# Kernel optimization log

Hardware: AMD Instinct MI355X
Metric: run time of the kernel (lower is better)

Reference implementation:

```python
import jax, jax.numpy as jnp
import numpy as np

UNITS = [100, 80, 50, 30]
D_IN = 64


def _lstm_layer(x, Wx, Wh, b):
    # x: [B, T, D]; Wx: [D, 4u]; Wh: [u, 4u]; b: [4u]
    B = x.shape[0]
    u = Wh.shape[0]
    # precompute input contribution for all timesteps: [B, T, 4u]
    xg = jnp.einsum('btd,dg->btg', x, Wx) + b

    def step(carry, xg_t):
        h, c = carry
        g = xg_t + h @ Wh                      # [B, 4u]
        i, f, cbar, o = jnp.split(g, 4, axis=-1)
        i = jax.nn.sigmoid(i)
        f = jax.nn.sigmoid(f)
        o = jax.nn.sigmoid(o)
        c = f * c + i * jnp.tanh(cbar)
        h = o * jnp.tanh(c)
        return (h, c), h

    init = (jnp.zeros((B, u), x.dtype), jnp.zeros((B, u), x.dtype))
    (h_final, _), hs = jax.lax.scan(step, init, jnp.swapaxes(xg, 0, 1))
    return jnp.swapaxes(hs, 0, 1), h_final  # [B, T, u], [B, u]


def setup_inputs() -> dict:
    key = jax.random.key(0)
    ks = jax.random.split(key, 16)
    B, T = 256, 1024
    inp = {"sequence": jax.random.normal(ks[0], (B, T, D_IN), dtype=jnp.float32)}
    d_in = D_IN
    for li, u in enumerate(UNITS):
        s_x = 1.0 / np.sqrt(d_in)
        s_h = 1.0 / np.sqrt(u)
        inp[f"Wx{li}"] = jax.random.normal(ks[1 + 3 * li], (d_in, 4 * u), dtype=jnp.float32) * s_x
        inp[f"Wh{li}"] = jax.random.normal(ks[2 + 3 * li], (u, 4 * u), dtype=jnp.float32) * s_h
        inp[f"b{li}"] = jnp.zeros((4 * u,), dtype=jnp.float32)
        d_in = u
    inp["W_out"] = jax.random.normal(ks[13], (UNITS[-1], 1), dtype=jnp.float32) / np.sqrt(UNITS[-1])
    inp["b_out"] = jnp.zeros((1,), dtype=jnp.float32)
    return inp


def reference(sequence, Wx0, Wh0, b0, Wx1, Wh1, b1, Wx2, Wh2, b2, Wx3, Wh3, b3, W_out, b_out):
    # 4 stacked LSTM layers; dropout is identity at inference.
    x, _ = _lstm_layer(sequence, Wx0, Wh0, b0)   # [B, T, 100]
    x, _ = _lstm_layer(x, Wx1, Wh1, b1)          # [B, T, 80]
    x, _ = _lstm_layer(x, Wx2, Wh2, b2)          # [B, T, 50]
    _, h = _lstm_layer(x, Wx3, Wh3, b3)          # final state [B, 30]
    return h @ W_out + b_out                     # [B, 1]
```

## Files before the change

kernel.cpp:

```cpp
#include <hip/hip_runtime.h>


#define BATCH 256
#define TFULL 1024
#define TC    128
#define NCHUNK (TFULL / TC)

__device__ __forceinline__ float fast_rcp(float x) {
    return __builtin_amdgcn_rcpf(x);
}

__device__ __forceinline__ float tanh_fast(float x) {
    float e = __expf(-2.0f * fabsf(x));
    float r = fast_rcp(1.0f + e);
    return copysignf(fmaf(2.0f, r, -1.0f), x);
}

__device__ __forceinline__ void lds_barrier() {
    asm volatile("s_waitcnt lgkmcnt(0)\n\ts_barrier" ::: "memory");
}

template<int CTRL>
__device__ __forceinline__ float dpp_add(float v) {
    int t = __builtin_amdgcn_update_dpp(0, __float_as_int(v), CTRL, 0xF, 0xF, true);
    return v + __int_as_float(t);
}
template<int CTRL>
__device__ __forceinline__ float dpp_mov(float v) {
    int t = __builtin_amdgcn_update_dpp(0, __float_as_int(v), CTRL, 0xF, 0xF, true);
    return __int_as_float(t);
}

template<int K, int N>
__global__ __launch_bounds__(256, 2)
void xg_gemm(const float* __restrict__ x, int batchStride,
             const float* __restrict__ Wx,
             const float* __restrict__ bias,
             float* __restrict__ out)
{
    constexpr int K4   = (K + 3) / 4;
    constexpr int SLAB = 64 * 4 + 4;

    const int n0   = blockIdx.x * 64;
    const int row0 = blockIdx.y * 64;
    const int tid  = threadIdx.x;
    const int tx   = tid & 15;
    const int ty   = tid >> 4;

    __shared__ __align__(16) float s_A[K4 * SLAB];
    __shared__ __align__(16) float s_B[K4 * 4 * 64];

    if constexpr ((K % 4) == 0) {
        for (int i = tid; i < 64 * (K / 4); i += 256) {
            const int row = i / (K / 4);
            const int k4  = i % (K / 4);
            const int gr  = row0 + row;
            const int b   = gr >> 7;
            const int t   = gr & 127;
            float4 v = *(const float4*)(x + (size_t)b * batchStride + t * K + k4 * 4);
            *(float4*)(s_A + k4 * SLAB + row * 4) = v;
        }
    } else {
        for (int i = tid; i < 64 * K; i += 256) {
            const int row = i / K;
            const int k   = i % K;
            const int gr  = row0 + row;
            const int b   = gr >> 7;
            const int t   = gr & 127;
            s_A[(k >> 2) * SLAB + row * 4 + (k & 3)] =
                x[(size_t)b * batchStride + t * K + k];
        }
        constexpr int PAD = K4 * 4 - K;
        for (int i = tid; i < 64 * PAD; i += 256) {
            const int row = i / PAD;
            const int kk  = K + i % PAD;
            s_A[(kk >> 2) * SLAB + row * 4 + (kk & 3)] = 0.0f;
        }
    }

    for (int i = tid; i < K4 * 4 * 16; i += 256) {
        const int k  = i >> 4;
        const int c4 = i & 15;
        float4 v = {0.0f, 0.0f, 0.0f, 0.0f};
        if (k < K && n0 + c4 * 4 < N)
            v = *(const float4*)(Wx + (size_t)k * N + n0 + c4 * 4);
        *(float4*)(s_B + k * 64 + c4 * 4) = v;
    }
    __syncthreads();

    float acc[4][4];
#pragma unroll
    for (int r = 0; r < 4; ++r)
#pragma unroll
        for (int c = 0; c < 4; ++c) acc[r][c] = 0.0f;

    for (int k4 = 0; k4 < K4; ++k4) {
        float4 bv[4];
#pragma unroll
        for (int j = 0; j < 4; ++j)
            bv[j] = *(const float4*)(s_B + (k4 * 4 + j) * 64 + tx * 4);
#pragma unroll
        for (int r = 0; r < 4; ++r) {
            float4 av = *(const float4*)(s_A + k4 * SLAB + (ty + 16 * r) * 4);
#pragma unroll
            for (int c = 0; c < 4; ++c) {
                acc[r][c] = fmaf(av.x, ((const float*)&bv[0])[c], acc[r][c]);
                acc[r][c] = fmaf(av.y, ((const float*)&bv[1])[c], acc[r][c]);
                acc[r][c] = fmaf(av.z, ((const float*)&bv[2])[c], acc[r][c]);
                acc[r][c] = fmaf(av.w, ((const float*)&bv[3])[c], acc[r][c]);
            }
        }
    }

    if (n0 + tx * 4 < N) {
        float4 bb = *(const float4*)(bias + n0 + tx * 4);
#pragma unroll
        for (int r = 0; r < 4; ++r) {
            float4 o;
            o.x = acc[r][0] + bb.x;
            o.y = acc[r][1] + bb.y;
            o.z = acc[r][2] + bb.z;
            o.w = acc[r][3] + bb.w;
            *(float4*)(out + (size_t)(row0 + ty + 16 * r) * N + n0 + tx * 4) = o;
        }
    }
}

template<int U, int S, int BLOCK, bool LAST>
__device__ __forceinline__ void rec_body(
    const float* __restrict__ xg,
    const float* __restrict__ Wh,
    float* __restrict__ xout,
    float* __restrict__ c_state,
    float* __restrict__ h_state,
    int first,
    const float* __restrict__ Wout,
    const float* __restrict__ bout,
    float* __restrict__ dout)
{
    constexpr int G = 4 * U;

    const int b   = blockIdx.x;
    const int tid = threadIdx.x;
    const int u   = tid >> 2;
    const int s   = tid & 3;
    const bool act_th = (u < U);
    const int uu  = act_th ? u : 0;

    __shared__ __align__(16) float s_h[2][4 * S];

    float w4[4][S];
#pragma unroll
    for (int g = 0; g < 4; ++g)
#pragma unroll
        for (int kk = 0; kk < S; ++kk) {
            const int k = s * S + kk;
            w4[g][kk] = (act_th && k < U) ? Wh[(size_t)k * G + g * U + uu] : 0.0f;
        }

    for (int i = tid; i < 2 * 4 * S; i += BLOCK) ((float*)s_h)[i] = 0.0f;
    __syncthreads();
    if (tid < U) s_h[0][tid] = first ? 0.0f : h_state[b * U + tid];
    float c = first ? 0.0f : c_state[b * U + uu];
    __syncthreads();

    const float* xgp = xg + (size_t)b * TC * G + (s * U + uu);
    float xg0 = xgp[0];
    float xg1 = xgp[G];

    int cur = 0;
    float h = 0.0f, hprev = 0.0f;
    const bool is_t = (s == 2);

    for (int t = 0; t < TC; ++t, cur ^= 1) {
        const int tp = (t + 2 < TC) ? (t + 2) : (TC - 1);
        const float xg2 = xgp[(size_t)tp * G];

        if (!LAST) {
            if (act_th && s == 0 && t > 0)
                xout[((size_t)b * TC + (t - 1)) * U + u] = hprev;
        }

        float a0 = 0.0f, a1 = 0.0f, a2 = 0.0f, a3 = 0.0f;
        const float* hs = &s_h[cur][s * S];
#pragma unroll
        for (int kk = 0; kk < S; kk += 4) {
            float4 v = *(const float4*)(hs + kk);
            a0 = fmaf(v.x, w4[0][kk + 0], a0);
            a0 = fmaf(v.y, w4[0][kk + 1], a0);
            a0 = fmaf(v.z, w4[0][kk + 2], a0);
            a0 = fmaf(v.w, w4[0][kk + 3], a0);
            a1 = fmaf(v.x, w4[1][kk + 0], a1);
            a1 = fmaf(v.y, w4[1][kk + 1], a1);
            a1 = fmaf(v.z, w4[1][kk + 2], a1);
            a1 = fmaf(v.w, w4[1][kk + 3], a1);
            a2 = fmaf(v.x, w4[2][kk + 0], a2);
            a2 = fmaf(v.y, w4[2][kk + 1], a2);
            a2 = fmaf(v.z, w4[2][kk + 2], a2);
            a2 = fmaf(v.w, w4[2][kk + 3], a2);
            a3 = fmaf(v.x, w4[3][kk + 0], a3);
            a3 = fmaf(v.y, w4[3][kk + 1], a3);
            a3 = fmaf(v.z, w4[3][kk + 2], a3);
            a3 = fmaf(v.w, w4[3][kk + 3], a3);
        }

        a0 = dpp_add<0xB1>(a0); a0 = dpp_add<0x4E>(a0);
        a1 = dpp_add<0xB1>(a1); a1 = dpp_add<0x4E>(a1);
        a2 = dpp_add<0xB1>(a2); a2 = dpp_add<0x4E>(a2);
        a3 = dpp_add<0xB1>(a3); a3 = dpp_add<0x4E>(a3);

        const float asum = (s == 0) ? a0 : (s == 1) ? a1 : (s == 2) ? a2 : a3;
        const float gs = asum + xg0;
        const float y  = is_t ? (-2.0f * fabsf(gs)) : (-gs);
        const float r  = fast_rcp(1.0f + __expf(y));
        const float v  = is_t ? copysignf(fmaf(2.0f, r, -1.0f), gs) : r;

        const float fi = dpp_mov<0x00>(v);
        const float ff = dpp_mov<0x55>(v);
        const float tc = dpp_mov<0xAA>(v);
        const float fo = dpp_mov<0xFF>(v);
        c = fmaf(ff, c, fi * tc);
        h = fo * tanh_fast(c);

        const int nxt = cur ^ 1;
        if (act_th && s == 0) s_h[nxt][u] = h;
        hprev = h;
        xg0 = xg1; xg1 = xg2;
        lds_barrier();
    }

    if (!LAST) {
        if (act_th && s == 0)
            xout[((size_t)b * TC + (TC - 1)) * U + u] = hprev;
    }
    if (act_th && s == 0) {
        c_state[b * U + u] = c;
        h_state[b * U + u] = h;
    }
    if (LAST && tid == 0) {
        float acc = bout[0];
#pragma unroll
        for (int k = 0; k < U; ++k) acc = fmaf(s_h[cur][k], Wout[k], acc);
        dout[b] = acc;
    }
}

#define REC_ARGS const float* __restrict__ xg, const float* __restrict__ Wh,        \
                 float* __restrict__ xout, float* __restrict__ c_state,             \
                 float* __restrict__ h_state, int first,                            \
                 const float* __restrict__ Wout, const float* __restrict__ bout,    \
                 float* __restrict__ dout
#define REC_PASS xg, Wh, xout, c_state, h_state, first, Wout, bout, dout

__attribute__((amdgpu_flat_work_group_size(448, 448), amdgpu_waves_per_eu(1, 2)))
__global__ void rec_l0(REC_ARGS) { rec_body<100, 28, 448, false>(REC_PASS); }

__attribute__((amdgpu_flat_work_group_size(320, 320), amdgpu_waves_per_eu(1, 2)))
__global__ void rec_l1(REC_ARGS) { rec_body<80, 20, 320, false>(REC_PASS); }

__attribute__((amdgpu_flat_work_group_size(256, 256), amdgpu_waves_per_eu(1, 2)))
__global__ void rec_l2(REC_ARGS) { rec_body<50, 16, 256, false>(REC_PASS); }

__attribute__((amdgpu_flat_work_group_size(128, 128), amdgpu_waves_per_eu(1, 2)))
__global__ void rec_l3(REC_ARGS) { rec_body<30, 8, 128, true>(REC_PASS); }

extern "C" void kernel_launch(void* const* d_in, const int* in_sizes, int n_in,
                              void* d_out, int out_size, void* d_ws, size_t ws_size,
                              hipStream_t stream)
{
    const float* seq  = (const float*)d_in[0];
    const float* Wx0  = (const float*)d_in[1];
    const float* Wh0  = (const float*)d_in[2];
    const float* b0   = (const float*)d_in[3];
    const float* Wx1  = (const float*)d_in[4];
    const float* Wh1  = (const float*)d_in[5];
    const float* b1   = (const float*)d_in[6];
    const float* Wx2  = (const float*)d_in[7];
    const float* Wh2  = (const float*)d_in[8];
    const float* b2   = (const float*)d_in[9];
    const float* Wx3  = (const float*)d_in[10];
    const float* Wh3  = (const float*)d_in[11];
    const float* b3   = (const float*)d_in[12];
    const float* Wout = (const float*)d_in[13];
    const float* bout = (const float*)d_in[14];
    float* out = (float*)d_out;

    const size_t XG_ELEMS = (size_t)BATCH * TC * 400;
    const size_t XC_ELEMS = (size_t)BATCH * TC * 100;
    float* ws  = (float*)d_ws;
    float* XGa = ws;
    float* XGb = XGa + XG_ELEMS;
    float* Xca = XGb + XG_ELEMS;
    float* Xcb = Xca + XC_ELEMS;
    float* st  = Xcb + XC_ELEMS;
    float* c0 = st + 0 * 32768; float* h0 = st + 1 * 32768;
    float* c1 = st + 2 * 32768; float* h1 = st + 3 * 32768;
    float* c2 = st + 4 * 32768; float* h2 = st + 5 * 32768;
    float* c3 = st + 6 * 32768; float* h3 = st + 7 * 32768;

    const dim3 gB(BATCH);

    for (int j = 0; j < NCHUNK; ++j) {
        const int first = (j == 0) ? 1 : 0;

        xg_gemm<64, 400><<<dim3(7, 512), 256, 0, stream>>>(
            seq + (size_t)j * TC * 64, TFULL * 64, Wx0, b0, XGa);
        rec_l0<<<gB, 448, 0, stream>>>(
            XGa, Wh0, Xca, c0, h0, first, nullptr, nullptr, nullptr);

        xg_gemm<100, 320><<<dim3(5, 512), 256, 0, stream>>>(
            Xca, TC * 100, Wx1, b1, XGb);
        rec_l1<<<gB, 320, 0, stream>>>(
            XGb, Wh1, Xcb, c1, h1, first, nullptr, nullptr, nullptr);

        xg_gemm<80, 200><<<dim3(4, 512), 256, 0, stream>>>(
            Xcb, TC * 80, Wx2, b2, XGa);
        rec_l2<<<gB, 256, 0, stream>>>(
            XGa, Wh2, Xca, c2, h2, first, nullptr, nullptr, nullptr);

        xg_gemm<50, 120><<<dim3(2, 512), 256, 0, stream>>>(
            Xca, TC * 50, Wx3, b3, XGb);
        rec_l3<<<gB, 128, 0, stream>>>(
            XGb, Wh3, nullptr, c3, h3, first, Wout, bout, out);
    }
}
```

Before: 2.870 ms.

## Pack two batch rows per recurrent workgroup and halve the grid

Each recurrence kernel now handles two batch sequences per workgroup. The two halves of the block keep separate double-buffered hidden-state arrays in LDS but share one barrier per timestep. The grid shrinks to 128 blocks, block sizes roughly double, and the waves_per_eu hints are dropped. The aim is to amortise per-block overhead, at the cost of larger barriers, possible register pressure from the per-thread weight arrays (with a risk of spills), and fewer active CUs.

New measurement: 3.930 ms. 36.9% more time.

```diff
diff --git a/kernel.cpp b/kernel.cpp
--- a/kernel.cpp
+++ b/kernel.cpp
@@ -126,7 +126,7 @@
     }
 }
 
-template<int U, int S, int BLOCK, bool LAST>
+template<int U, int S, int HBLK, bool LAST>
 __device__ __forceinline__ void rec_body(
     const float* __restrict__ xg,
     const float* __restrict__ Wh,
@@ -138,16 +138,19 @@
     const float* __restrict__ bout,
     float* __restrict__ dout)
 {
-    constexpr int G = 4 * U;
-
-    const int b   = blockIdx.x;
-    const int tid = threadIdx.x;
-    const int u   = tid >> 2;
-    const int s   = tid & 3;
+    constexpr int G     = 4 * U;
+    constexpr int BLOCK = 2 * HBLK;
+
+    const int tid  = threadIdx.x;
+    const int half = (tid >= HBLK) ? 1 : 0;
+    const int tin  = tid - half * HBLK;
+    const int b    = blockIdx.x * 2 + half;
+    const int u    = tin >> 2;
+    const int s    = tin & 3;
     const bool act_th = (u < U);
-    const int uu  = act_th ? u : 0;
-
-    __shared__ __align__(16) float s_h[2][4 * S];
+    const int uu   = act_th ? u : 0;
+
+    __shared__ __align__(16) float s_h[2][2][4 * S];
 
     float w4[4][S];
 #pragma unroll
@@ -158,9 +161,9 @@
             w4[g][kk] = (act_th && k < U) ? Wh[(size_t)k * G + g * U + uu] : 0.0f;
         }
 
-    for (int i = tid; i < 2 * 4 * S; i += BLOCK) ((float*)s_h)[i] = 0.0f;
+    for (int i = tid; i < 2 * 2 * 4 * S; i += BLOCK) ((float*)s_h)[i] = 0.0f;
     __syncthreads();
-    if (tid < U) s_h[0][tid] = first ? 0.0f : h_state[b * U + tid];
+    if (tin < U) s_h[half][0][tin] = first ? 0.0f : h_state[b * U + tin];
     float c = first ? 0.0f : c_state[b * U + uu];
     __syncthreads();
 
@@ -182,7 +185,7 @@
         }
 
         float a0 = 0.0f, a1 = 0.0f, a2 = 0.0f, a3 = 0.0f;
-        const float* hs = &s_h[cur][s * S];
+        const float* hs = &s_h[half][cur][s * S];
 #pragma unroll
         for (int kk = 0; kk < S; kk += 4) {
             float4 v = *(const float4*)(hs + kk);
@@ -223,7 +226,7 @@
         h = fo * tanh_fast(c);
 
         const int nxt = cur ^ 1;
-        if (act_th && s == 0) s_h[nxt][u] = h;
+        if (act_th && s == 0) s_h[half][nxt][u] = h;
         hprev = h;
         xg0 = xg1; xg1 = xg2;
         lds_barrier();
@@ -237,10 +240,10 @@
         c_state[b * U + u] = c;
         h_state[b * U + u] = h;
     }
-    if (LAST && tid == 0) {
+    if (LAST && tin == 0) {
         float acc = bout[0];
 #pragma unroll
-        for (int k = 0; k < U; ++k) acc = fmaf(s_h[cur][k], Wout[k], acc);
+        for (int k = 0; k < U; ++k) acc = fmaf(s_h[half][cur][k], Wout[k], acc);
         dout[b] = acc;
     }
 }
@@ -252,16 +255,16 @@
                  float* __restrict__ dout
 #define REC_PASS xg, Wh, xout, c_state, h_state, first, Wout, bout, dout
 
-__attribute__((amdgpu_flat_work_group_size(448, 448), amdgpu_waves_per_eu(1, 2)))
-__global__ void rec_l0(REC_ARGS) { rec_body<100, 28, 448, false>(REC_PASS); }
-
-__attribute__((amdgpu_flat_work_group_size(320, 320), amdgpu_waves_per_eu(1, 2)))
+__attribute__((amdgpu_flat_work_group_size(800, 800)))
+__global__ void rec_l0(REC_ARGS) { rec_body<100, 28, 400, false>(REC_PASS); }
+
+__attribute__((amdgpu_flat_work_group_size(640, 640)))
 __global__ void rec_l1(REC_ARGS) { rec_body<80, 20, 320, false>(REC_PASS); }
 
-__attribute__((amdgpu_flat_work_group_size(256, 256), amdgpu_waves_per_eu(1, 2)))
-__global__ void rec_l2(REC_ARGS) { rec_body<50, 16, 256, false>(REC_PASS); }
-
-__attribute__((amdgpu_flat_work_group_size(128, 128), amdgpu_waves_per_eu(1, 2)))
+__attribute__((amdgpu_flat_work_group_size(416, 416)))
+__global__ void rec_l2(REC_ARGS) { rec_body<50, 16, 208, false>(REC_PASS); }
+
+__attribute__((amdgpu_flat_work_group_size(256, 256)))
 __global__ void rec_l3(REC_ARGS) { rec_body<30, 8, 128, true>(REC_PASS); }
 
 extern "C" void kernel_launch(void* const* d_in, const int* in_sizes, int n_in,
@@ -298,29 +301,29 @@
     float* c2 = st + 4 * 32768; float* h2 = st + 5 * 32768;
     float* c3 = st + 6 * 32768; float* h3 = st + 7 * 32768;
 
-    const dim3 gB(BATCH);
+    const dim3 gB(BATCH / 2);
 
     for (int j = 0; j < NCHUNK; ++j) {
         const int first = (j == 0) ? 1 : 0;
 
         xg_gemm<64, 400><<<dim3(7, 512), 256, 0, stream>>>(
             seq + (size_t)j * TC * 64, TFULL * 64, Wx0, b0, XGa);
-        rec_l0<<<gB, 448, 0, stream>>>(
+        rec_l0<<<gB, 800, 0, stream>>>(
             XGa, Wh0, Xca, c0, h0, first, nullptr, nullptr, nullptr);
 
         xg_gemm<100, 320><<<dim3(5, 512), 256, 0, stream>>>(
             Xca, TC * 100, Wx1, b1, XGb);
-        rec_l1<<<gB, 320, 0, stream>>>(
+        rec_l1<<<gB, 640, 0, stream>>>(
             XGb, Wh1, Xcb, c1, h1, first, nullptr, nullptr, nullptr);
 
         xg_gemm<80, 200><<<dim3(4, 512), 256, 0, stream>>>(
             Xcb, TC * 80, Wx2, b2, XGa);
-        rec_l2<<<gB, 256, 0, stream>>>(
+        rec_l2<<<gB, 416, 0, stream>>>(
             XGa, Wh2, Xca, c2, h2, first, nullptr, nullptr, nullptr);
 
         xg_gemm<50, 120><<<dim3(2, 512), 256, 0, stream>>>(
             Xca, TC * 50, Wx3, b3, XGb);
-        rec_l3<<<gB, 128, 0, stream>>>(
+        rec_l3<<<gB, 256, 0, stream>>>(
             XGb, Wh3, nullptr, c3, h3, first, Wout, bout, out);
     }
 }
```

## Process two batch rows per recurrent block to share weights and overlap chains

Applied to the files above, without the earlier changes.

Each recurrent LSTM block now handles two batch sequences instead of one, with the grid halved to BATCH/2. The register-resident Wh weights are reused for both sequences, and the two independent dependency chains are interleaved, so per-step latency and the per-step LDS barrier are spread over twice the work. The waves_per_eu hint is dropped to allow more registers. In exchange only 128 blocks launch, leaving many CUs idle, and each step carries more arithmetic and more register pressure.

Result: slower. 4.103 ms (+43.0%).

```diff
diff --git a/kernel.cpp b/kernel.cpp
--- a/kernel.cpp
+++ b/kernel.cpp
@@ -140,14 +140,15 @@
 {
     constexpr int G = 4 * U;
 
-    const int b   = blockIdx.x;
     const int tid = threadIdx.x;
+    const int b0  = blockIdx.x * 2;
+    const int b1  = b0 + 1;
     const int u   = tid >> 2;
     const int s   = tid & 3;
     const bool act_th = (u < U);
     const int uu  = act_th ? u : 0;
 
-    __shared__ __align__(16) float s_h[2][4 * S];
+    __shared__ __align__(16) float s_h[2][2][4 * S];
 
     float w4[4][S];
 #pragma unroll
@@ -158,90 +159,135 @@
             w4[g][kk] = (act_th && k < U) ? Wh[(size_t)k * G + g * U + uu] : 0.0f;
         }
 
-    for (int i = tid; i < 2 * 4 * S; i += BLOCK) ((float*)s_h)[i] = 0.0f;
+    for (int i = tid; i < 2 * 2 * 4 * S; i += BLOCK) ((float*)s_h)[i] = 0.0f;
     __syncthreads();
-    if (tid < U) s_h[0][tid] = first ? 0.0f : h_state[b * U + tid];
-    float c = first ? 0.0f : c_state[b * U + uu];
+    if (tid < U)               s_h[0][0][tid]     = first ? 0.0f : h_state[b0 * U + tid];
+    else if (tid < 2 * U)      s_h[1][0][tid - U] = first ? 0.0f : h_state[b1 * U + (tid - U)];
+    float c0 = first ? 0.0f : c_state[b0 * U + uu];
+    float c1 = first ? 0.0f : c_state[b1 * U + uu];
     __syncthreads();
 
-    const float* xgp = xg + (size_t)b * TC * G + (s * U + uu);
-    float xg0 = xgp[0];
-    float xg1 = xgp[G];
+    const float* xgp0 = xg + (size_t)b0 * TC * G + (s * U + uu);
+    const float* xgp1 = xg + (size_t)b1 * TC * G + (s * U + uu);
+    float xa0 = xgp0[0], xa1 = xgp0[G];
+    float xb0 = xgp1[0], xb1 = xgp1[G];
 
     int cur = 0;
-    float h = 0.0f, hprev = 0.0f;
+    float h0v = 0.0f, h1v = 0.0f, hp0 = 0.0f, hp1 = 0.0f;
     const bool is_t = (s == 2);
 
     for (int t = 0; t < TC; ++t, cur ^= 1) {
         const int tp = (t + 2 < TC) ? (t + 2) : (TC - 1);
-        const float xg2 = xgp[(size_t)tp * G];
+        const float xa2 = xgp0[(size_t)tp * G];
+        const float xb2 = xgp1[(size_t)tp * G];
 
         if (!LAST) {
-            if (act_th && s == 0 && t > 0)
-                xout[((size_t)b * TC + (t - 1)) * U + u] = hprev;
-        }
-
-        float a0 = 0.0f, a1 = 0.0f, a2 = 0.0f, a3 = 0.0f;
-        const float* hs = &s_h[cur][s * S];
+            if (act_th && s == 0 && t > 0) {
+                xout[((size_t)b0 * TC + (t - 1)) * U + u] = hp0;
+                xout[((size_t)b1 * TC + (t - 1)) * U + u] = hp1;
+            }
+        }
+
+        float p0 = 0.0f, p1 = 0.0f, p2 = 0.0f, p3 = 0.0f;
+        float q0 = 0.0f, q1 = 0.0f, q2 = 0.0f, q3 = 0.0f;
+        const float* hsA = &s_h[0][cur][s * S];
+        const float* hsB = &s_h[1][cur][s * S];
 #pragma unroll
         for (int kk = 0; kk < S; kk += 4) {
-            float4 v = *(const float4*)(hs + kk);
-            a0 = fmaf(v.x, w4[0][kk + 0], a0);
-            a0 = fmaf(v.y, w4[0][kk + 1], a0);
-            a0 = fmaf(v.z, w4[0][kk + 2], a0);
-            a0 = fmaf(v.w, w4[0][kk + 3], a0);
-            a1 = fmaf(v.x, w4[1][kk + 0], a1);
-            a1 = fmaf(v.y, w4[1][kk + 1], a1);
-            a1 = fmaf(v.z, w4[1][kk + 2], a1);
-            a1 = fmaf(v.w, w4[1][kk + 3], a1);
-            a2 = fmaf(v.x, w4[2][kk + 0], a2);
-            a2 = fmaf(v.y, w4[2][kk + 1], a2);
-            a2 = fmaf(v.z, w4[2][kk + 2], a2);
-            a2 = fmaf(v.w, w4[2][kk + 3], a2);
-            a3 = fmaf(v.x, w4[3][kk + 0], a3);
-            a3 = fmaf(v.y, w4[3][kk + 1], a3);
-            a3 = fmaf(v.z, w4[3][kk + 2], a3);
-            a3 = fmaf(v.w, w4[3][kk + 3], a3);
-        }
-
-        a0 = dpp_add<0xB1>(a0); a0 = dpp_add<0x4E>(a0);
-        a1 = dpp_add<0xB1>(a1); a1 = dpp_add<0x4E>(a1);
-        a2 = dpp_add<0xB1>(a2); a2 = dpp_add<0x4E>(a2);
-        a3 = dpp_add<0xB1>(a3); a3 = dpp_add<0x4E>(a3);
-
-        const float asum = (s == 0) ? a0 : (s == 1) ? a1 : (s == 2) ? a2 : a3;
-        const float gs = asum + xg0;
-        const float y  = is_t ? (-2.0f * fabsf(gs)) : (-gs);
-        const float r  = fast_rcp(1.0f + __expf(y));
-        const float v  = is_t ? copysignf(fmaf(2.0f, r, -1.0f), gs) : r;
-
-        const float fi = dpp_mov<0x00>(v);
-        const float ff = dpp_mov<0x55>(v);
-        const float tc = dpp_mov<0xAA>(v);
-        const float fo = dpp_mov<0xFF>(v);
-        c = fmaf(ff, c, fi * tc);
-        h = fo * tanh_fast(c);
+            float4 va = *(const float4*)(hsA + kk);
+            float4 vb = *(const float4*)(hsB + kk);
+            p0 = fmaf(va.x, w4[0][kk + 0], p0);
+            q0 = fmaf(vb.x, w4[0][kk + 0], q0);
+            p0 = fmaf(va.y, w4[0][kk + 1], p0);
+            q0 = fmaf(vb.y, w4[0][kk + 1], q0);
+            p0 = fmaf(va.z, w4[0][kk + 2], p0);
+            q0 = fmaf(vb.z, w4[0][kk + 2], q0);
+            p0 = fmaf(va.w, w4[0][kk + 3], p0);
+            q0 = fmaf(vb.w, w4[0][kk + 3], q0);
+            p1 = fmaf(va.x, w4[1][kk + 0], p1);
+            q1 = fmaf(vb.x, w4[1][kk + 0], q1);
+            p1 = fmaf(va.y, w4[1][kk + 1], p1);
+            q1 = fmaf(vb.y, w4[1][kk + 1], q1);
+            p1 = fmaf(va.z, w4[1][kk + 2], p1);
+            q1 = fmaf(vb.z, w4[1][kk + 2], q1);
+            p1 = fmaf(va.w, w4[1][kk + 3], p1);
+            q1 = fmaf(vb.w, w4[1][kk + 3], q1);
+            p2 = fmaf(va.x, w4[2][kk + 0], p2);
+            q2 = fmaf(vb.x, w4[2][kk + 0], q2);
+            p2 = fmaf(va.y, w4[2][kk + 1], p2);
+            q2 = fmaf(vb.y, w4[2][kk + 1], q2);
+            p2 = fmaf(va.z, w4[2][kk + 2], p2);
+            q2 = fmaf(vb.z, w4[2][kk + 2], q2);
+            p2 = fmaf(va.w, w4[2][kk + 3], p2);
+            q2 = fmaf(vb.w, w4[2][kk + 3], q2);
+            p3 = fmaf(va.x, w4[3][kk + 0], p3);
+            q3 = fmaf(vb.x, w4[3][kk + 0], q3);
+            p3 = fmaf(va.y, w4[3][kk + 1], p3);
+            q3 = fmaf(vb.y, w4[3][kk + 1], q3);
+            p3 = fmaf(va.z, w4[3][kk + 2], p3);
+            q3 = fmaf(vb.z, w4[3][kk + 2], q3);
+            p3 = fmaf(va.w, w4[3][kk + 3], p3);
+            q3 = fmaf(vb.w, w4[3][kk + 3], q3);
+        }
+
+        p0 = dpp_add<0xB1>(p0); q0 = dpp_add<0xB1>(q0);
+        p1 = dpp_add<0xB1>(p1); q1 = dpp_add<0xB1>(q1);
+        p2 = dpp_add<0xB1>(p2); q2 = dpp_add<0xB1>(q2);
+        p3 = dpp_add<0xB1>(p3); q3 = dpp_add<0xB1>(q3);
+        p0 = dpp_add<0x4E>(p0); q0 = dpp_add<0x4E>(q0);
+        p1 = dpp_add<0x4E>(p1); q1 = dpp_add<0x4E>(q1);
+        p2 = dpp_add<0x4E>(p2); q2 = dpp_add<0x4E>(q2);
+        p3 = dpp_add<0x4E>(p3); q3 = dpp_add<0x4E>(q3);
+
+        const float pa = (s == 0) ? p0 : (s == 1) ? p1 : (s == 2) ? p2 : p3;
+        const float qa = (s == 0) ? q0 : (s == 1) ? q1 : (s == 2) ? q2 : q3;
+        const float gsa = pa + xa0;
+        const float gsb = qa + xb0;
+        const float ya  = is_t ? (-2.0f * fabsf(gsa)) : (-gsa);
+        const float yb  = is_t ? (-2.0f * fabsf(gsb)) : (-gsb);
+        const float ra  = fast_rcp(1.0f + __expf(ya));
+        const float rb  = fast_rcp(1.0f + __expf(yb));
+        const float va  = is_t ? copysignf(fmaf(2.0f, ra, -1.0f), gsa) : ra;
+        const float vb  = is_t ? copysignf(fmaf(2.0f, rb, -1.0f), gsb) : rb;
+
+        const float fia = dpp_mov<0x00>(va), fib = dpp_mov<0x00>(vb);
+        const float ffa = dpp_mov<0x55>(va), ffb = dpp_mov<0x55>(vb);
+        const float tca = dpp_mov<0xAA>(va), tcb = dpp_mov<0xAA>(vb);
+        const float foa = dpp_mov<0xFF>(va), fob = dpp_mov<0xFF>(vb);
+        c0 = fmaf(ffa, c0, fia * tca);
+        c1 = fmaf(ffb, c1, fib * tcb);
+        h0v = foa * tanh_fast(c0);
+        h1v = fob * tanh_fast(c1);
 
         const int nxt = cur ^ 1;
-        if (act_th && s == 0) s_h[nxt][u] = h;
-        hprev = h;
-        xg0 = xg1; xg1 = xg2;
+        if (act_th && s == 0) {
+            s_h[0][nxt][u] = h0v;
+            s_h[1][nxt][u] = h1v;
+        }
+        hp0 = h0v; hp1 = h1v;
+        xa0 = xa1; xa1 = xa2;
+        xb0 = xb1; xb1 = xb2;
         lds_barrier();
     }
 
     if (!LAST) {
-        if (act_th && s == 0)
-            xout[((size_t)b * TC + (TC - 1)) * U + u] = hprev;
+        if (act_th && s == 0) {
+            xout[((size_t)b0 * TC + (TC - 1)) * U + u] = hp0;
+            xout[((size_t)b1 * TC + (TC - 1)) * U + u] = hp1;
+        }
     }
     if (act_th && s == 0) {
-        c_state[b * U + u] = c;
-        h_state[b * U + u] = h;
-    }
-    if (LAST && tid == 0) {
+        c_state[b0 * U + u] = c0;
+        h_state[b0 * U + u] = h0v;
+        c_state[b1 * U + u] = c1;
+        h_state[b1 * U + u] = h1v;
+    }
+    if (LAST && tid < 2) {
+        const float* hh = s_h[tid][cur];
         float acc = bout[0];
 #pragma unroll
-        for (int k = 0; k < U; ++k) acc = fmaf(s_h[cur][k], Wout[k], acc);
-        dout[b] = acc;
+        for (int k = 0; k < U; ++k) acc = fmaf(hh[k], Wout[k], acc);
+        dout[b0 + tid] = acc;
     }
 }
 
@@ -252,16 +298,16 @@
                  float* __restrict__ dout
 #define REC_PASS xg, Wh, xout, c_state, h_state, first, Wout, bout, dout
 
-__attribute__((amdgpu_flat_work_group_size(448, 448), amdgpu_waves_per_eu(1, 2)))
+__attribute__((amdgpu_flat_work_group_size(448, 448)))
 __global__ void rec_l0(REC_ARGS) { rec_body<100, 28, 448, false>(REC_PASS); }
 
-__attribute__((amdgpu_flat_work_group_size(320, 320), amdgpu_waves_per_eu(1, 2)))
+__attribute__((amdgpu_flat_work_group_size(320, 320)))
 __global__ void rec_l1(REC_ARGS) { rec_body<80, 20, 320, false>(REC_PASS); }
 
-__attribute__((amdgpu_flat_work_group_size(256, 256), amdgpu_waves_per_eu(1, 2)))
+__attribute__((amdgpu_flat_work_group_size(256, 256)))
 __global__ void rec_l2(REC_ARGS) { rec_body<50, 16, 256, false>(REC_PASS); }
 
-__attribute__((amdgpu_flat_work_group_size(128, 128), amdgpu_waves_per_eu(1, 2)))
+__attribute__((amdgpu_flat_work_group_size(128, 128)))
 __global__ void rec_l3(REC_ARGS) { rec_body<30, 8, 128, true>(REC_PASS); }
 
 extern "C" void kernel_launch(void* const* d_in, const int* in_sizes, int n_in,
@@ -298,7 +344,7 @@
     float* c2 = st + 4 * 32768; float* h2 = st + 5 * 32768;
     float* c3 = st + 6 * 32768; float* h3 = st + 7 * 32768;
 
-    const dim3 gB(BATCH);
+    const dim3 gB(BATCH / 2);
 
     for (int j = 0; j < NCHUNK; ++j) {
         const int first = (j == 0) ? 1 : 0;
```
